# Optimization experiments

Hardware: AMD Instinct MI355X
Metric: run time of the kernel (lower is better)

## Reference

```python
import jax, jax.numpy as jnp
import numpy as np

B, N, A, H, HID = 2048, 8, 16, 32, 64   # batch, n_agents, dim_action, dim_utility_hidden, dim_hidden
DQ = (H + A) * N                         # dim_q_input


def setup_inputs() -> dict:
    key = jax.random.key(0)
    ks = jax.random.split(key, 6)
    def w(k, shape, fan_in):
        return jax.random.normal(k, shape, jnp.float32) / np.sqrt(fan_in).astype(np.float32)
    return {
        "hidden_states_n": jax.random.normal(ks[0], (B, N, H), jnp.float32),
        # one-hot actions, as QTRAN substitutes torch.eye(dim_action) rows
        "actions_n": jax.nn.one_hot(jax.random.randint(ks[1], (B, N), 0, A), A, dtype=jnp.float32),
        "q_w1": w(ks[2], (DQ, HID), DQ), "q_b1": jnp.zeros((HID,), jnp.float32),
        "q_w2": w(ks[3], (HID, HID), HID), "q_b2": jnp.zeros((HID,), jnp.float32),
        "q_w3": w(ks[4], (HID, 1), HID), "q_b3": jnp.zeros((1,), jnp.float32),
    }


def reference(hidden_states_n, actions_n, q_w1, q_b1, q_w2, q_b2, q_w3, q_b3):
    """Vectorized QTRAN_alt.counterfactual_values_hat.

    Original: for each agent g and action a, replace agent g's action with one-hot(a)
    and run the joint Q_jt MLP. Here all n_agents*dim_action substitutions are
    built by broadcasting and run as one batched MLP.
    Output: [B, n_agents, dim_action].
    """
    Bn, Nn, Hh = hidden_states_n.shape
    Aa = actions_n.shape[-1]
    eye_a = jnp.eye(Aa, dtype=actions_n.dtype)          # [a, dA]
    agent_eq = jnp.eye(Nn, dtype=bool)                  # [g, j]: j == g
    # cf_actions[b, g, a, j, :] = eye_a[a] if j == g else actions_n[b, j, :]
    cf_actions = jnp.where(
        agent_eq[None, :, None, :, None],               # [1,G,1,J,1]
        eye_a[None, None, :, None, :],                  # [1,1,A,1,dA]
        actions_n[:, None, None, :, :],                 # [B,1,1,J,dA]
    )                                                   # [B,G,A,J,dA]
    hid = jnp.broadcast_to(hidden_states_n[:, None, None, :, :], (Bn, Nn, Aa, Nn, Hh))
    # per-agent (hidden, action) concat then flatten agents, matching
    # torch.cat([h, a], -1).view([-1, dim_q_input])
    inp = jnp.concatenate([hid, cf_actions], axis=-1).reshape(Bn, Nn, Aa, Nn * (Hh + Aa))
    h1 = jax.nn.relu(inp @ q_w1 + q_b1)
    h2 = jax.nn.relu(h1 @ q_w2 + q_b2)
    q = h2 @ q_w3 + q_b3                                # [B, G, A, 1]
    return q[..., 0]
```

## Files before the change

### kernel.cpp

```cpp
#include <hip/hip_runtime.h>
#include <hip/hip_bf16.h>

typedef __attribute__((ext_vector_type(4))) float f32x4;
typedef __attribute__((ext_vector_type(8))) short bf16x8;
typedef __attribute__((ext_vector_type(4))) short s16x4;

#define H1S 72

struct Smem {
    float inp[384];
    float base[64];
    float sub[8][64];
    int   sel[8];
    union {
        float part[4][64];
        __align__(16) short h1[128 * H1S];
    } u;
};

template<bool ISF32>
__device__ __forceinline__ float ldin(const void* p, int i) {
    if constexpr (ISF32) return ((const float*)p)[i];
    else return __bfloat162float(((const __hip_bfloat16*)p)[i]);
}

template<bool ISF32>
__device__ __forceinline__ f32x4 ldq(const void* p, int i) {
    if constexpr (ISF32) return *(const f32x4*)((const float*)p + i);
    else {
        const __hip_bfloat16* q = (const __hip_bfloat16*)p + i;
        return (f32x4){__bfloat162float(q[0]), __bfloat162float(q[1]),
                       __bfloat162float(q[2]), __bfloat162float(q[3])};
    }
}

__device__ __forceinline__ short bf16bits(float v) {
    __hip_bfloat16 h = __float2bfloat16(v);
    return *(const short*)&h;
}
__device__ __forceinline__ float bf16val(short s) {
    return __bfloat162float(*(const __hip_bfloat16*)&s);
}

__device__ __forceinline__ bool word_looks_bf16(unsigned int w) {
    const unsigned int lo = w & 0xFFFFu;
    const unsigned int ex = (lo >> 7) & 0xFFu;
    return (ex >= 100u && ex <= 140u) || (lo & 0x7FFFu) == 0u;
}

__device__ __forceinline__ bool vote_isf32_scalar(const void* hidden) {
    const unsigned int* hw = (const unsigned int*)hidden;
    int cnt = 0;
    #pragma unroll
    for (int i = 0; i < 32; ++i) cnt += word_looks_bf16(hw[i]) ? 1 : 0;
    return cnt < 16;
}

template<bool ISF32>
__device__ void w2prep_body(const void* w2, short* wsfrag, int idx0) {
    #pragma unroll
    for (int i = 0; i < 2; ++i) {
        const int idx = idx0 + i * 2048;
        const int j = idx & 7;
        const int lane = (idx >> 3) & 63;
        const int nt = (idx >> 9) & 3;
        const int ks = idx >> 11;
        const int src = (ks * 32 + (lane >> 4) * 8 + j) * 64 + nt * 16 + (lane & 15);
        const float v = ldin<ISF32>(w2, src);
        const short hb = bf16bits(v);
        wsfrag[idx] = hb;
        wsfrag[4096 + idx] = bf16bits(v - bf16val(hb));
    }
}

__global__ __launch_bounds__(256) void w2prep_kernel(
    const void* __restrict__ hidden, const void* __restrict__ w2,
    short* __restrict__ wsfrag) {
    const int idx0 = blockIdx.x * 256 + threadIdx.x;
    if (vote_isf32_scalar(hidden)) w2prep_body<true>(w2, wsfrag, idx0);
    else                           w2prep_body<false>(w2, wsfrag, idx0);
}

template<bool ISF32, bool W2D>
__device__ void qtran_body(Smem& sm,
    const void* __restrict__ hidden, const void* __restrict__ actions,
    const void* __restrict__ w1, const void* __restrict__ b1,
    const void* __restrict__ w2, const void* __restrict__ b2,
    const void* __restrict__ w3, const void* __restrict__ b3,
    void* __restrict__ out, const short* __restrict__ wsfrag, int b, int t)
{
    const int lane = t & 63;
    const int wv = t >> 6;
    const int q = lane >> 4;
    const int n = lane & 15;
    const int fq = lane & 15;
    const int rofs = lane >> 4;

    if (t < 64) {
        const int j = t >> 3, k4 = (t & 7) * 4;
        *(f32x4*)&sm.inp[j * 48 + k4] = ldq<ISF32>(hidden, (b * 8 + j) * 32 + k4);
    } else if (t < 96) {
        const int i = t - 64;
        const int j = i >> 2, c4 = (i & 3) * 4;
        *(f32x4*)&sm.inp[j * 48 + 32 + c4] = ldq<ISF32>(actions, (b * 8 + j) * 16 + c4);
    }
    __syncthreads();

    if (t < 128) {
        const int g = t >> 4, a = t & 15;
        if (sm.inp[g * 48 + 32 + a] > 0.5f) sm.sel[g] = a;
    }

    {
        f32x4 a4 = (f32x4){0.f, 0.f, 0.f, 0.f};
        #pragma unroll 8
        for (int p = 0; p < 16; ++p) {
            const int hr = wv * 64 + p * 4 + rofs;
            const int r = (hr >> 5) * 48 + (hr & 31);
            const float xv = sm.inp[r];
            const f32x4 wq = ldq<ISF32>(w1, r * 64 + fq * 4);
            #pragma unroll
            for (int c = 0; c < 4; ++c) a4[c] = fmaf(xv, wq[c], a4[c]);
        }
        #pragma unroll
        for (int c = 0; c < 4; ++c) {
            a4[c] += __shfl_xor(a4[c], 16);
            a4[c] += __shfl_xor(a4[c], 32);
        }
        if (rofs == 0) *(f32x4*)&sm.u.part[wv][fq * 4] = a4;
    }
    __syncthreads();

    if (t < 128) {
        const int g = t >> 4, f4 = (t & 15) * 4;
        *(f32x4*)&sm.sub[g][f4] =
            ldq<ISF32>(w1, (g * 48 + 32 + sm.sel[g]) * 64 + f4);
    } else if (t < 192) {
        const int f = t - 128;
        sm.base[f] = ldin<ISF32>(b1, f) + sm.u.part[0][f] + sm.u.part[1][f]
                   + sm.u.part[2][f] + sm.u.part[3][f];
    }
    __syncthreads();

    {
        const int itm = t >> 4;
        const int hfq = t & 15;
        f32x4 S = *(const f32x4*)&sm.sub[0][hfq * 4];
        #pragma unroll
        for (int g = 1; g < 8; ++g) {
            const f32x4 sg = *(const f32x4*)&sm.sub[g][hfq * 4];
            #pragma unroll
            for (int c = 0; c < 4; ++c) S[c] += sg[c];
        }
        f32x4 bs = *(const f32x4*)&sm.base[hfq * 4];
        #pragma unroll
        for (int c = 0; c < 4; ++c) bs[c] += S[c];
        #pragma unroll
        for (int p = 0; p < 8; ++p) {
            const int item = p * 16 + itm;
            const int g = item >> 4, a = item & 15;
            const f32x4 wq = ldq<ISF32>(w1, (g * 48 + 32 + a) * 64 + hfq * 4);
            const f32x4 sb = *(const f32x4*)&sm.sub[g][hfq * 4];
            s16x4 hi;
            #pragma unroll
            for (int c = 0; c < 4; ++c)
                hi[c] = bf16bits(fmaxf(bs[c] - sb[c] + wq[c], 0.f));
            *(s16x4*)&sm.u.h1[item * H1S + hfq * 4] = hi;
        }
    }
    __syncthreads();

    f32x4 acc[2][4];
    #pragma unroll
    for (int mt = 0; mt < 2; ++mt)
      #pragma unroll
      for (int nt = 0; nt < 4; ++nt)
        acc[mt][nt] = (f32x4){0.f, 0.f, 0.f, 0.f};

    #pragma unroll
    for (int ks = 0; ks < 2; ++ks) {
        bf16x8 ahi[2];
        #pragma unroll
        for (int mt = 0; mt < 2; ++mt) {
            const int item = wv * 32 + mt * 16 + n;
            ahi[mt] = *(const bf16x8*)&sm.u.h1[item * H1S + ks * 32 + q * 8];
        }
        bf16x8 bhi[4], blo[4];
        if constexpr (!W2D) {
            #pragma unroll
            for (int nt = 0; nt < 4; ++nt) {
                const int fb = ((ks * 4 + nt) * 64 + lane) * 8;
                bhi[nt] = *(const bf16x8*)&wsfrag[fb];
                blo[nt] = *(const bf16x8*)&wsfrag[4096 + fb];
            }
        } else {
            #pragma unroll
            for (int nt = 0; nt < 4; ++nt)
                #pragma unroll
                for (int j = 0; j < 8; ++j) {
                    const float v = ldin<ISF32>(w2, (ks * 32 + q * 8 + j) * 64 + nt * 16 + n);
                    const short hb = bf16bits(v);
                    bhi[nt][j] = hb;
                    blo[nt][j] = bf16bits(v - bf16val(hb));
                }
        }
        #pragma unroll
        for (int nt = 0; nt < 4; ++nt)
            #pragma unroll
            for (int mt = 0; mt < 2; ++mt) {
                acc[mt][nt] = __builtin_amdgcn_mfma_f32_16x16x32_bf16(
                    ahi[mt], bhi[nt], acc[mt][nt], 0, 0, 0);
                acc[mt][nt] = __builtin_amdgcn_mfma_f32_16x16x32_bf16(
                    ahi[mt], blo[nt], acc[mt][nt], 0, 0, 0);
            }
    }

    float b2f[4], w3f[4];
    #pragma unroll
    for (int nt = 0; nt < 4; ++nt) {
        b2f[nt] = ldin<ISF32>(b2, nt * 16 + n);
        w3f[nt] = ldin<ISF32>(w3, nt * 16 + n);
    }
    const float b3f = ldin<ISF32>(b3, 0);

    #pragma unroll
    for (int mt = 0; mt < 2; ++mt) {
      #pragma unroll
      for (int r = 0; r < 4; ++r) {
        float p = 0.f;
        #pragma unroll
        for (int nt = 0; nt < 4; ++nt) {
            const float h2 = fmaxf(acc[mt][nt][r] + b2f[nt], 0.f);
            p = fmaf(h2, w3f[nt], p);
        }
        p += __shfl_xor(p, 1);
        p += __shfl_xor(p, 2);
        p += __shfl_xor(p, 4);
        p += __shfl_xor(p, 8);
        if (n == mt * 4 + r) {
            const int item = wv * 32 + mt * 16 + q * 4 + r;
            if constexpr (ISF32) ((float*)out)[b * 128 + item] = p + b3f;
            else ((__hip_bfloat16*)out)[b * 128 + item] = __float2bfloat16(p + b3f);
        }
      }
    }
}

template<bool W2D>
__global__ __launch_bounds__(256, 4) void qtran_cf_kernel(
    const void* __restrict__ hidden, const void* __restrict__ actions,
    const void* __restrict__ w1, const void* __restrict__ b1,
    const void* __restrict__ w2, const void* __restrict__ b2,
    const void* __restrict__ w3, const void* __restrict__ b3,
    void* __restrict__ out, const short* __restrict__ wsfrag)
{
    __shared__ Smem sm;
    const unsigned int* hw = (const unsigned int*)hidden;
    const bool pass = word_looks_bf16(hw[threadIdx.x & 31]);
    const unsigned long long m = __ballot(pass);
    const bool isf32 = (__popcll(m) < 32);

    const int b = blockIdx.x;
    const int t = threadIdx.x;
    if (isf32)
        qtran_body<true, W2D>(sm, hidden, actions, w1, b1, w2, b2, w3, b3, out, wsfrag, b, t);
    else
        qtran_body<false, W2D>(sm, hidden, actions, w1, b1, w2, b2, w3, b3, out, wsfrag, b, t);
}

extern "C" void kernel_launch(void* const* d_in, const int* in_sizes, int n_in,
                              void* d_out, int out_size, void* d_ws, size_t ws_size,
                              hipStream_t stream) {
    short* wsfrag = (ws_size >= 16384) ? (short*)d_ws : nullptr;
    if (wsfrag) {
        w2prep_kernel<<<8, 256, 0, stream>>>(d_in[0], d_in[4], wsfrag);
        qtran_cf_kernel<false><<<2048, 256, 0, stream>>>(
            d_in[0], d_in[1], d_in[2], d_in[3], d_in[4], d_in[5], d_in[6], d_in[7],
            d_out, wsfrag);
    } else {
        qtran_cf_kernel<true><<<2048, 256, 0, stream>>>(
            d_in[0], d_in[1], d_in[2], d_in[3], d_in[4], d_in[5], d_in[6], d_in[7],
            d_out, nullptr);
    }
}
```

Measured before the change: 85.51 us.

## Split into per-batch correction kernel and MFMA layer-2 kernel via workspace

Splits the work into two kernels. Kernel A handles four batch items per block: it computes the layer-1 base sum, subtracts each agent's selected-action row, writes the per-agent corrections to the workspace, and also folds in the W2 bf16 hi/lo fragment prep. Kernel B then builds the h1 tile directly in registers by adding the matching W1 action row to each correction, skipping the old shared-memory h1 staging. The aim is to share W1 loads across several batch items and shorten the main kernel, at the cost of a 4 MB workspace round trip and a required workspace size. A fused fallback kernel is kept for when the workspace is too small.

Result: slower. 89.88 us (+5.1%).

```diff
diff --git a/kernel.cpp b/kernel.cpp
--- a/kernel.cpp
+++ b/kernel.cpp
@@ -5,18 +5,8 @@
 typedef __attribute__((ext_vector_type(8))) short bf16x8;
 typedef __attribute__((ext_vector_type(4))) short s16x4;
 
-#define H1S 72
-
-struct Smem {
-    float inp[384];
-    float base[64];
-    float sub[8][64];
-    int   sel[8];
-    union {
-        float part[4][64];
-        __align__(16) short h1[128 * H1S];
-    } u;
-};
+#define NB 4
+#define CORR_OFF_F 4096
 
 template<bool ISF32>
 __device__ __forceinline__ float ldin(const void* p, int i) {
@@ -48,12 +38,11 @@
     return (ex >= 100u && ex <= 140u) || (lo & 0x7FFFu) == 0u;
 }
 
-__device__ __forceinline__ bool vote_isf32_scalar(const void* hidden) {
+__device__ __forceinline__ bool vote_isf32(const void* hidden, int t) {
     const unsigned int* hw = (const unsigned int*)hidden;
-    int cnt = 0;
-    #pragma unroll
-    for (int i = 0; i < 32; ++i) cnt += word_looks_bf16(hw[i]) ? 1 : 0;
-    return cnt < 16;
+    const bool pass = word_looks_bf16(hw[t & 31]);
+    const unsigned long long m = __ballot(pass);
+    return __popcll(m) < 32;
 }
 
 template<bool ISF32>
@@ -73,21 +62,263 @@
     }
 }
 
-__global__ __launch_bounds__(256) void w2prep_kernel(
-    const void* __restrict__ hidden, const void* __restrict__ w2,
-    short* __restrict__ wsfrag) {
-    const int idx0 = blockIdx.x * 256 + threadIdx.x;
-    if (vote_isf32_scalar(hidden)) w2prep_body<true>(w2, wsfrag, idx0);
-    else                           w2prep_body<false>(w2, wsfrag, idx0);
-}
-
-template<bool ISF32, bool W2D>
-__device__ void qtran_body(Smem& sm,
+struct SmemA {
+    float inp[NB][384];
+    float part[4][NB][64];
+    float baseAll[NB][64];
+    float sub[NB][8][64];
+    int   sel[NB][8];
+};
+
+template<bool ISF32>
+__device__ void qtranA_body(SmemA& sm,
+    const void* __restrict__ hidden, const void* __restrict__ actions,
+    const void* __restrict__ w1, const void* __restrict__ b1,
+    const void* __restrict__ w2, float* __restrict__ ws, int blk, int t)
+{
+    const int lane = t & 63;
+    const int wv = t >> 6;
+    const int fq = lane & 15;
+    const int rofs = lane >> 4;
+    const int b0 = blk * NB;
+
+    {
+        const int i0 = t >> 6, s = t & 63;
+        const int j = s >> 3, k4 = (s & 7) * 4;
+        *(f32x4*)&sm.inp[i0][j * 48 + k4] =
+            ldq<ISF32>(hidden, ((b0 + i0) * 8 + j) * 32 + k4);
+        if (s < 32) {
+            const int ja = s >> 2, c4 = (s & 3) * 4;
+            *(f32x4*)&sm.inp[i0][ja * 48 + 32 + c4] =
+                ldq<ISF32>(actions, ((b0 + i0) * 8 + ja) * 16 + c4);
+        }
+    }
+    __syncthreads();
+
+    {
+        const int i0 = t >> 6, s = t & 63, a = s & 15;
+        const int g1 = s >> 4;
+        if (sm.inp[i0][g1 * 48 + 32 + a] > 0.5f) sm.sel[i0][g1] = a;
+        const int g2 = g1 + 4;
+        if (sm.inp[i0][g2 * 48 + 32 + a] > 0.5f) sm.sel[i0][g2] = a;
+    }
+
+    {
+        f32x4 a4[NB];
+        #pragma unroll
+        for (int i = 0; i < NB; ++i) a4[i] = (f32x4){0.f, 0.f, 0.f, 0.f};
+        #pragma unroll 8
+        for (int p = 0; p < 16; ++p) {
+            const int hr = wv * 64 + p * 4 + rofs;
+            const int r = (hr >> 5) * 48 + (hr & 31);
+            const f32x4 wq = ldq<ISF32>(w1, r * 64 + fq * 4);
+            #pragma unroll
+            for (int i = 0; i < NB; ++i) {
+                const float xv = sm.inp[i][r];
+                #pragma unroll
+                for (int c = 0; c < 4; ++c) a4[i][c] = fmaf(xv, wq[c], a4[i][c]);
+            }
+        }
+        #pragma unroll
+        for (int i = 0; i < NB; ++i)
+          #pragma unroll
+          for (int c = 0; c < 4; ++c) {
+            a4[i][c] += __shfl_xor(a4[i][c], 16);
+            a4[i][c] += __shfl_xor(a4[i][c], 32);
+          }
+        if (rofs == 0) {
+            #pragma unroll
+            for (int i = 0; i < NB; ++i)
+                *(f32x4*)&sm.part[wv][i][fq * 4] = a4[i];
+        }
+    }
+    __syncthreads();
+
+    #pragma unroll
+    for (int p = 0; p < 2; ++p) {
+        const int idx = p * 256 + t;
+        const int i = idx >> 7, g = (idx >> 4) & 7, qd = idx & 15;
+        *(f32x4*)&sm.sub[i][g][qd * 4] =
+            ldq<ISF32>(w1, (g * 48 + 32 + sm.sel[i][g]) * 64 + qd * 4);
+    }
+    __syncthreads();
+
+    {
+        const int i = t >> 6, f = t & 63;
+        float v = ldin<ISF32>(b1, f);
+        #pragma unroll
+        for (int w = 0; w < 4; ++w) v += sm.part[w][i][f];
+        #pragma unroll
+        for (int g = 0; g < 8; ++g) v += sm.sub[i][g][f];
+        sm.baseAll[i][f] = v;
+    }
+    __syncthreads();
+
+    #pragma unroll
+    for (int p = 0; p < 2; ++p) {
+        const int idx = p * 256 + t;
+        const int i = idx >> 7, g = (idx >> 4) & 7, qd = idx & 15;
+        const f32x4 ba = *(const f32x4*)&sm.baseAll[i][qd * 4];
+        const f32x4 sb = *(const f32x4*)&sm.sub[i][g][qd * 4];
+        const f32x4 c = (f32x4){ba[0] - sb[0], ba[1] - sb[1],
+                                ba[2] - sb[2], ba[3] - sb[3]};
+        *(f32x4*)&ws[CORR_OFF_F + ((b0 + i) * 8 + g) * 64 + qd * 4] = c;
+    }
+
+    if (blk < 8)
+        w2prep_body<ISF32>(w2, (short*)ws, blk * 256 + t);
+}
+
+__global__ __launch_bounds__(256, 2) void qtranA_kernel(
+    const void* __restrict__ hidden, const void* __restrict__ actions,
+    const void* __restrict__ w1, const void* __restrict__ b1,
+    const void* __restrict__ w2, float* __restrict__ ws)
+{
+    __shared__ SmemA sm;
+    const int t = threadIdx.x;
+    if (vote_isf32(hidden, t))
+        qtranA_body<true>(sm, hidden, actions, w1, b1, w2, ws, blockIdx.x, t);
+    else
+        qtranA_body<false>(sm, hidden, actions, w1, b1, w2, ws, blockIdx.x, t);
+}
+
+template<bool ISF32>
+__device__ void qtranB_body(float (&corr_s)[8][64],
+    const void* __restrict__ w1, const void* __restrict__ b2,
+    const void* __restrict__ w3, const void* __restrict__ b3,
+    void* __restrict__ out, const float* __restrict__ ws, int b, int t)
+{
+    const int lane = t & 63;
+    const int wv = t >> 6;
+    const int q = lane >> 4;
+    const int n = lane & 15;
+
+    f32x4 wr[2][2][2];
+    #pragma unroll
+    for (int mt = 0; mt < 2; ++mt) {
+        const int row = ((wv * 2 + mt) * 48 + 32 + n) * 64;
+        #pragma unroll
+        for (int ks = 0; ks < 2; ++ks) {
+            wr[mt][ks][0] = ldq<ISF32>(w1, row + ks * 32 + q * 8);
+            wr[mt][ks][1] = ldq<ISF32>(w1, row + ks * 32 + q * 8 + 4);
+        }
+    }
+    float b2f[4], w3f[4];
+    #pragma unroll
+    for (int nt = 0; nt < 4; ++nt) {
+        b2f[nt] = ldin<ISF32>(b2, nt * 16 + n);
+        w3f[nt] = ldin<ISF32>(w3, nt * 16 + n);
+    }
+    const float b3f = ldin<ISF32>(b3, 0);
+
+    if (t < 128) {
+        const int g = t >> 4, qd = t & 15;
+        *(f32x4*)&corr_s[g][qd * 4] =
+            *(const f32x4*)&ws[CORR_OFF_F + (b * 8 + g) * 64 + qd * 4];
+    }
+    __syncthreads();
+
+    bf16x8 af[2][2];
+    #pragma unroll
+    for (int mt = 0; mt < 2; ++mt) {
+        const int g = wv * 2 + mt;
+        #pragma unroll
+        for (int ks = 0; ks < 2; ++ks)
+          #pragma unroll
+          for (int h = 0; h < 2; ++h) {
+            const int f0 = ks * 32 + q * 8 + h * 4;
+            const f32x4 cc = *(const f32x4*)&corr_s[g][f0];
+            const f32x4 w4 = wr[mt][ks][h];
+            #pragma unroll
+            for (int c = 0; c < 4; ++c)
+                af[ks][mt][h * 4 + c] = bf16bits(fmaxf(cc[c] + w4[c], 0.f));
+          }
+    }
+
+    f32x4 acc[2][4];
+    #pragma unroll
+    for (int mt = 0; mt < 2; ++mt)
+      #pragma unroll
+      for (int nt = 0; nt < 4; ++nt)
+        acc[mt][nt] = (f32x4){0.f, 0.f, 0.f, 0.f};
+
+    const short* wsfrag = (const short*)ws;
+    #pragma unroll
+    for (int ks = 0; ks < 2; ++ks) {
+        bf16x8 bhi[4], blo[4];
+        #pragma unroll
+        for (int nt = 0; nt < 4; ++nt) {
+            const int fb = ((ks * 4 + nt) * 64 + lane) * 8;
+            bhi[nt] = *(const bf16x8*)&wsfrag[fb];
+            blo[nt] = *(const bf16x8*)&wsfrag[4096 + fb];
+        }
+        #pragma unroll
+        for (int nt = 0; nt < 4; ++nt)
+          #pragma unroll
+          for (int mt = 0; mt < 2; ++mt) {
+            acc[mt][nt] = __builtin_amdgcn_mfma_f32_16x16x32_bf16(
+                af[ks][mt], bhi[nt], acc[mt][nt], 0, 0, 0);
+            acc[mt][nt] = __builtin_amdgcn_mfma_f32_16x16x32_bf16(
+                af[ks][mt], blo[nt], acc[mt][nt], 0, 0, 0);
+          }
+    }
+
+    #pragma unroll
+    for (int mt = 0; mt < 2; ++mt) {
+      #pragma unroll
+      for (int r = 0; r < 4; ++r) {
+        float p = 0.f;
+        #pragma unroll
+        for (int nt = 0; nt < 4; ++nt) {
+            const float h2 = fmaxf(acc[mt][nt][r] + b2f[nt], 0.f);
+            p = fmaf(h2, w3f[nt], p);
+        }
+        p += __shfl_xor(p, 1);
+        p += __shfl_xor(p, 2);
+        p += __shfl_xor(p, 4);
+        p += __shfl_xor(p, 8);
+        if (n == mt * 4 + r) {
+            const int item = wv * 32 + mt * 16 + q * 4 + r;
+            if constexpr (ISF32) ((float*)out)[b * 128 + item] = p + b3f;
+            else ((__hip_bfloat16*)out)[b * 128 + item] = __float2bfloat16(p + b3f);
+        }
+      }
+    }
+}
+
+__global__ __launch_bounds__(256, 4) void qtranB_kernel(
+    const void* __restrict__ hidden,
+    const void* __restrict__ w1, const void* __restrict__ b2,
+    const void* __restrict__ w3, const void* __restrict__ b3,
+    void* __restrict__ out, const float* __restrict__ ws)
+{
+    __shared__ float corr_s[8][64];
+    const int t = threadIdx.x;
+    if (vote_isf32(hidden, t))
+        qtranB_body<true>(corr_s, w1, b2, w3, b3, out, ws, blockIdx.x, t);
+    else
+        qtranB_body<false>(corr_s, w1, b2, w3, b3, out, ws, blockIdx.x, t);
+}
+
+#define H1S 72
+struct SmemM {
+    float inp[384];
+    float base[64];
+    float sub[8][64];
+    int   sel[8];
+    union {
+        float part[4][64];
+        __align__(16) short h1[128 * H1S];
+    } u;
+};
+
+template<bool ISF32>
+__device__ void qtranM_body(SmemM& sm,
     const void* __restrict__ hidden, const void* __restrict__ actions,
     const void* __restrict__ w1, const void* __restrict__ b1,
     const void* __restrict__ w2, const void* __restrict__ b2,
     const void* __restrict__ w3, const void* __restrict__ b3,
-    void* __restrict__ out, const short* __restrict__ wsfrag, int b, int t)
+    void* __restrict__ out, int b, int t)
 {
     const int lane = t & 63;
     const int wv = t >> 6;
@@ -110,7 +341,6 @@
         const int g = t >> 4, a = t & 15;
         if (sm.inp[g * 48 + 32 + a] > 0.5f) sm.sel[g] = a;
     }
-
     {
         f32x4 a4 = (f32x4){0.f, 0.f, 0.f, 0.f};
         #pragma unroll 8
@@ -186,24 +416,15 @@
             ahi[mt] = *(const bf16x8*)&sm.u.h1[item * H1S + ks * 32 + q * 8];
         }
         bf16x8 bhi[4], blo[4];
-        if constexpr (!W2D) {
-            #pragma unroll
-            for (int nt = 0; nt < 4; ++nt) {
-                const int fb = ((ks * 4 + nt) * 64 + lane) * 8;
-                bhi[nt] = *(const bf16x8*)&wsfrag[fb];
-                blo[nt] = *(const bf16x8*)&wsfrag[4096 + fb];
+        #pragma unroll
+        for (int nt = 0; nt < 4; ++nt)
+            #pragma unroll
+            for (int j = 0; j < 8; ++j) {
+                const float v = ldin<ISF32>(w2, (ks * 32 + q * 8 + j) * 64 + nt * 16 + n);
+                const short hb = bf16bits(v);
+                bhi[nt][j] = hb;
+                blo[nt][j] = bf16bits(v - bf16val(hb));
             }
-        } else {
-            #pragma unroll
-            for (int nt = 0; nt < 4; ++nt)
-                #pragma unroll
-                for (int j = 0; j < 8; ++j) {
-                    const float v = ldin<ISF32>(w2, (ks * 32 + q * 8 + j) * 64 + nt * 16 + n);
-                    const short hb = bf16bits(v);
-                    bhi[nt][j] = hb;
-                    blo[nt][j] = bf16bits(v - bf16val(hb));
-                }
-        }
         #pragma unroll
         for (int nt = 0; nt < 4; ++nt)
             #pragma unroll
@@ -246,40 +467,36 @@
     }
 }
 
-template<bool W2D>
-__global__ __launch_bounds__(256, 4) void qtran_cf_kernel(
+__global__ __launch_bounds__(256, 4) void qtranM_kernel(
     const void* __restrict__ hidden, const void* __restrict__ actions,
     const void* __restrict__ w1, const void* __restrict__ b1,
     const void* __restrict__ w2, const void* __restrict__ b2,
     const void* __restrict__ w3, const void* __restrict__ b3,
-    void* __restrict__ out, const short* __restrict__ wsfrag)
+    void* __restrict__ out)
 {
-    __shared__ Smem sm;
-    const unsigned int* hw = (const unsigned int*)hidden;
-    const bool pass = word_looks_bf16(hw[threadIdx.x & 31]);
-    const unsigned long long m = __ballot(pass);
-    const bool isf32 = (__popcll(m) < 32);
-
-    const int b = blockIdx.x;
+    __shared__ SmemM sm;
     const int t = threadIdx.x;
-    if (isf32)
-        qtran_body<true, W2D>(sm, hidden, actions, w1, b1, w2, b2, w3, b3, out, wsfrag, b, t);
+    if (vote_isf32(hidden, t))
+        qtranM_body<true>(sm, hidden, actions, w1, b1, w2, b2, w3, b3, out,
+                          blockIdx.x, t);
     else
-        qtran_body<false, W2D>(sm, hidden, actions, w1, b1, w2, b2, w3, b3, out, wsfrag, b, t);
+        qtranM_body<false>(sm, hidden, actions, w1, b1, w2, b2, w3, b3, out,
+                           blockIdx.x, t);
 }
 
 extern "C" void kernel_launch(void* const* d_in, const int* in_sizes, int n_in,
                               void* d_out, int out_size, void* d_ws, size_t ws_size,
                               hipStream_t stream) {
-    short* wsfrag = (ws_size >= 16384) ? (short*)d_ws : nullptr;
-    if (wsfrag) {
-        w2prep_kernel<<<8, 256, 0, stream>>>(d_in[0], d_in[4], wsfrag);
-        qtran_cf_kernel<false><<<2048, 256, 0, stream>>>(
+    const size_t need = 16384 + (size_t)2048 * 8 * 64 * 4;
+    if (ws_size >= need) {
+        float* ws = (float*)d_ws;
+        qtranA_kernel<<<512, 256, 0, stream>>>(
+            d_in[0], d_in[1], d_in[2], d_in[3], d_in[4], ws);
+        qtranB_kernel<<<2048, 256, 0, stream>>>(
+            d_in[0], d_in[2], d_in[5], d_in[6], d_in[7], d_out, ws);
+    } else {
+        qtranM_kernel<<<2048, 256, 0, stream>>>(
             d_in[0], d_in[1], d_in[2], d_in[3], d_in[4], d_in[5], d_in[6], d_in[7],
-            d_out, wsfrag);
-    } else {
-        qtran_cf_kernel<true><<<2048, 256, 0, stream>>>(
-            d_in[0], d_in[1], d_in[2], d_in[3], d_in[4], d_in[5], d_in[6], d_in[7],
-            d_out, nullptr);
-    }
-}
+            d_out);
+    }
+}
```
